# Kernel tuning notes

Hardware: AMD Instinct MI355X
Metric: run time of the kernel (lower is better)

Reference implementation:

```python
import jax, jax.numpy as jnp
import numpy as np

N = 100000
E = 1600000
F_IN, F_HID, F_OUT = 128, 256, 16


def gcn_conv(x, edge_index, W, b, num_nodes):
    """PyG-style GCNConv: out = D^{-1/2} (A + I) D^{-1/2} (x W) + b."""
    src, dst = edge_index[0], edge_index[1]
    # add self-loops
    loops = jnp.arange(num_nodes, dtype=edge_index.dtype)
    src = jnp.concatenate([src, loops])
    dst = jnp.concatenate([dst, loops])
    # degree of destination nodes (includes self-loop, so deg >= 1)
    deg = jax.ops.segment_sum(jnp.ones_like(dst, dtype=x.dtype), dst, num_segments=num_nodes)
    dinv = jax.lax.rsqrt(deg)
    norm = dinv[src] * dinv[dst]  # [E+N]
    h = x @ W                      # [N, out]  dense transform first (PyG order)
    msg = h[src] * norm[:, None]   # gather + scale, [E+N, out]
    out = jax.ops.segment_sum(msg, dst, num_segments=num_nodes)  # scatter-add
    return out + b


def setup_inputs() -> dict:
    key = jax.random.key(0)
    k1, k2, k3, k4 = jax.random.split(key, 4)
    x = jax.random.normal(k1, (N, F_IN), dtype=jnp.float32)
    edge_index = jax.random.randint(k2, (2, E), 0, N, dtype=jnp.int64)
    # Glorot-ish init for weights
    W1 = jax.random.normal(k3, (F_IN, F_HID), dtype=jnp.float32) / np.sqrt(F_IN)
    W2 = jax.random.normal(k4, (F_HID, F_OUT), dtype=jnp.float32) / np.sqrt(F_HID)
    b1 = jnp.zeros((F_HID,), dtype=jnp.float32)
    b2 = jnp.zeros((F_OUT,), dtype=jnp.float32)
    return {"x": x, "edge_index": edge_index, "W1": W1, "b1": b1, "W2": W2, "b2": b2}


def reference(x, edge_index, W1, b1, W2, b2):
    h = gcn_conv(x, edge_index, W1, b1, N)
    h = jax.nn.relu(h)
    # dropout p=0.5 is identity in eval mode
    h = gcn_conv(h, edge_index, W2, b2, N)
    return jax.nn.log_softmax(h, axis=1)
```

## Files before the change

kernel.cpp:

```cpp
#include <hip/hip_runtime.h>
#include <hip/hip_bf16.h>

#define F_IN   128
#define F_HID  256
#define F_OUT  16
#define NCH    256
#define MAXBUK 1600

__device__ inline unsigned short f2bf(float x) {
    unsigned int u = __float_as_uint(x);
    unsigned int r = (u + 0x7FFFu + ((u >> 16) & 1u)) >> 16;
    return (unsigned short)r;
}
__device__ inline unsigned int pack2(float lo, float hi) {
    return (unsigned int)f2bf(lo) | ((unsigned int)f2bf(hi) << 16);
}
__device__ inline void unpack8(uint4 v, float* f) {
    f[0] = __uint_as_float(v.x << 16); f[1] = __uint_as_float(v.x & 0xFFFF0000u);
    f[2] = __uint_as_float(v.y << 16); f[3] = __uint_as_float(v.y & 0xFFFF0000u);
    f[4] = __uint_as_float(v.z << 16); f[5] = __uint_as_float(v.z & 0xFFFF0000u);
    f[6] = __uint_as_float(v.w << 16); f[7] = __uint_as_float(v.w & 0xFFFF0000u);
}

__global__ __launch_bounds__(256) void hist_k(const int* __restrict__ ei,
                                              int* __restrict__ M,
                                              int E, int cpe, int nbuk) {
    __shared__ int h[MAXBUK];
    int tid = threadIdx.x, blk = blockIdx.x;
    for (int b = tid; b < nbuk; b += 256) h[b] = 0;
    __syncthreads();
    int e0 = blk * cpe;
    for (int i = tid; i < cpe; i += 256) {
        int e = e0 + i;
        if (e < E) atomicAdd(&h[ei[E + e] >> 6], 1);
    }
    __syncthreads();
    for (int b = tid; b < nbuk; b += 256) M[(size_t)blk * nbuk + b] = h[b];
}

__global__ __launch_bounds__(64) void colscan_k(int* __restrict__ M,
                                                int* __restrict__ totals,
                                                int nbuk) {
    int b = blockIdx.x, l = threadIdx.x;
    int v[4], s = 0;
    #pragma unroll
    for (int u = 0; u < 4; ++u) { v[u] = M[(size_t)(l * 4 + u) * nbuk + b]; s += v[u]; }
    int incl = s;
    #pragma unroll
    for (int o = 1; o < 64; o <<= 1) { int t = __shfl_up(incl, o); if (l >= o) incl += t; }
    int run = incl - s;
    #pragma unroll
    for (int u = 0; u < 4; ++u) { M[(size_t)(l * 4 + u) * nbuk + b] = run; run += v[u]; }
    if (l == 63) totals[b] = incl;
}

__global__ __launch_bounds__(1024) void base_k(const int* __restrict__ totals,
                                               int* __restrict__ base, int nbuk) {
    __shared__ int sm[1024];
    int t = threadIdx.x;
    int v0 = (2 * t     < nbuk) ? totals[2 * t]     : 0;
    int v1 = (2 * t + 1 < nbuk) ? totals[2 * t + 1] : 0;
    int p = v0 + v1;
    sm[t] = p;
    __syncthreads();
    for (int o = 1; o < 1024; o <<= 1) {
        int x = (t >= o) ? sm[t - o] : 0;
        __syncthreads();
        sm[t] += x;
        __syncthreads();
    }
    int excl = sm[t] - p;
    if (2 * t     < nbuk) base[2 * t]     = excl;
    if (2 * t + 1 < nbuk) base[2 * t + 1] = excl + v0;
}

__global__ __launch_bounds__(256) void bscatter_k(const int* __restrict__ ei,
                                                  const int* __restrict__ M,
                                                  const int* __restrict__ base,
                                                  int2* __restrict__ tmp,
                                                  int E, int cpe, int nbuk) {
    __shared__ int cur[MAXBUK];
    int tid = threadIdx.x, blk = blockIdx.x;
    for (int b = tid; b < nbuk; b += 256)
        cur[b] = base[b] + M[(size_t)blk * nbuk + b];
    __syncthreads();
    int e0 = blk * cpe;
    for (int i = tid; i < cpe; i += 256) {
        int e = e0 + i;
        if (e < E) {
            int s = ei[e], d = ei[E + e];
            int slot = atomicAdd(&cur[d >> 6], 1);
            tmp[slot] = make_int2(s, d);
        }
    }
}

__global__ __launch_bounds__(256) void fin_k(const int2* __restrict__ tmp,
                                             const int* __restrict__ base,
                                             const int* __restrict__ totals,
                                             const float* __restrict__ x,
                                             int* __restrict__ csr_src,
                                             int* __restrict__ start,
                                             int* __restrict__ deg,
                                             float* __restrict__ dinv,
                                             uint4* __restrict__ xs,
                                             int N) {
    __shared__ int dcnt[64], dcur[64];
    __shared__ float sdv[64];
    int b = blockIdx.x, tid = threadIdx.x;
    int bb = base[b], cnt = totals[b];
    if (tid < 64) dcnt[tid] = 0;
    __syncthreads();
    for (int i = tid; i < cnt; i += 256)
        atomicAdd(&dcnt[tmp[bb + i].y & 63], 1);
    __syncthreads();
    if (tid < 64) {
        int l = tid, v = dcnt[l];
        int incl = v;
        #pragma unroll
        for (int o = 1; o < 64; o <<= 1) { int t2 = __shfl_up(incl, o); if (l >= o) incl += t2; }
        int excl = incl - v;
        dcur[l] = excl;
        float dv = rsqrtf((float)v + 1.f);
        sdv[l] = dv;
        int d = b * 64 + l;
        if (d < N) { deg[d] = v; start[d] = bb + excl; dinv[d] = dv; }
    }
    __syncthreads();
    for (int i = tid; i < cnt; i += 256) {
        int2 p = tmp[bb + i];
        int r = atomicAdd(&dcur[p.y & 63], 1);
        csr_src[bb + r] = p.x;
    }
    int d0 = b * 64;
    int nn = min(64, N - d0);
    const float4* x4 = (const float4*)x;
    for (int i = tid; i < nn * 16; i += 256) {
        int l = i >> 4, c = i & 15;
        float dv = sdv[l];
        size_t f4i = (size_t)(d0 + l) * 32 + c * 2;
        float4 a = x4[f4i], bq = x4[f4i + 1];
        a.x *= dv; a.y *= dv; a.z *= dv; a.w *= dv;
        bq.x *= dv; bq.y *= dv; bq.z *= dv; bq.w *= dv;
        uint4 o;
        o.x = pack2(a.x, a.y);  o.y = pack2(a.z, a.w);
        o.z = pack2(bq.x, bq.y); o.w = pack2(bq.z, bq.w);
        xs[(size_t)(d0 + l) * 16 + c] = o;
    }
}

__global__ __launch_bounds__(256) void agg1_k(const uint4* __restrict__ xs,
                                              const float* __restrict__ dinv,
                                              const int* __restrict__ start,
                                              const int* __restrict__ deg,
                                              const int* __restrict__ csr_src,
                                              float* __restrict__ agg1,
                                              int N) {
    int wid = (blockIdx.x * 256 + threadIdx.x) >> 6;
    if (wid >= N) return;
    int lane = threadIdx.x & 63;
    int q  = lane >> 4;
    int li = lane & 15;

    float acc[8];
    {
        uint4 self = xs[(size_t)wid * 16 + li];
        float f[8]; unpack8(self, f);
        float sw = (q == 0) ? 1.f : 0.f;
        #pragma unroll
        for (int j = 0; j < 8; ++j) acc[j] = f[j] * sw;
    }

    int s0 = start[wid], cnt = deg[wid];
    for (int p = 0; p < cnt; p += 16) {
        int s[4]; float nm[4]; uint4 v[4];
        #pragma unroll
        for (int u = 0; u < 4; ++u) {
            int e = p + u * 4 + q;
            s[u]  = (e < cnt) ? csr_src[s0 + e] : wid;
            nm[u] = (e < cnt) ? 1.f : 0.f;
        }
        #pragma unroll
        for (int u = 0; u < 4; ++u)
            v[u] = xs[(size_t)s[u] * 16 + li];
        #pragma unroll
        for (int u = 0; u < 4; ++u) {
            float f[8]; unpack8(v[u], f);
            #pragma unroll
            for (int j = 0; j < 8; ++j) acc[j] = fmaf(f[j], nm[u], acc[j]);
        }
    }
    #pragma unroll
    for (int j = 0; j < 8; ++j) {
        acc[j] += __shfl_xor(acc[j], 16);
        acc[j] += __shfl_xor(acc[j], 32);
    }
    if (q == 0) {
        float dv = dinv[wid];
        float4 o0 = { acc[0] * dv, acc[1] * dv, acc[2] * dv, acc[3] * dv };
        float4 o1 = { acc[4] * dv, acc[5] * dv, acc[6] * dv, acc[7] * dv };
        ((float4*)agg1)[(size_t)wid * 32 + li * 2 + 0] = o0;
        ((float4*)agg1)[(size_t)wid * 32 + li * 2 + 1] = o1;
    }
}

#define BM 64
#define BN 64
#define BK 16

__global__ __launch_bounds__(256) void gemm1_relu_k(const float* __restrict__ A,
                                                    const float* __restrict__ B,
                                                    const float* __restrict__ bias,
                                                    float* __restrict__ C,
                                                    int M_) {
    __shared__ float As[BK][BM + 4];
    __shared__ float Bs[BK][BN + 4];
    int m0 = blockIdx.x * BM;
    int n0 = blockIdx.y * BN;
    int tid = threadIdx.x;
    int tx = tid & 15, ty = tid >> 4;
    float acc[4][4] = {};

    for (int k0 = 0; k0 < F_IN; k0 += BK) {
        {
            int r = tid >> 2, kk = (tid & 3) * 4;
            int row = m0 + r; if (row >= M_) row = M_ - 1;
            float4 av = *reinterpret_cast<const float4*>(A + (size_t)row * F_IN + k0 + kk);
            As[kk + 0][r] = av.x; As[kk + 1][r] = av.y;
            As[kk + 2][r] = av.z; As[kk + 3][r] = av.w;
        }
        {
            int k = tid >> 4, nn = (tid & 15) * 4;
            float4 bv = *reinterpret_cast<const float4*>(B + (size_t)(k0 + k) * F_HID + n0 + nn);
            *reinterpret_cast<float4*>(&Bs[k][nn]) = bv;
        }
        __syncthreads();
        #pragma unroll
        for (int kk = 0; kk < BK; ++kk) {
            float4 a = *reinterpret_cast<const float4*>(&As[kk][ty * 4]);
            float4 b = *reinterpret_cast<const float4*>(&Bs[kk][tx * 4]);
            acc[0][0] += a.x * b.x; acc[0][1] += a.x * b.y; acc[0][2] += a.x * b.z; acc[0][3] += a.x * b.w;
            acc[1][0] += a.y * b.x; acc[1][1] += a.y * b.y; acc[1][2] += a.y * b.z; acc[1][3] += a.y * b.w;
            acc[2][0] += a.z * b.x; acc[2][1] += a.z * b.y; acc[2][2] += a.z * b.z; acc[2][3] += a.z * b.w;
            acc[3][0] += a.w * b.x; acc[3][1] += a.w * b.y; acc[3][2] += a.w * b.z; acc[3][3] += a.w * b.w;
        }
        __syncthreads();
    }
    #pragma unroll
    for (int i = 0; i < 4; ++i) {
        int row = m0 + ty * 4 + i;
        if (row < M_) {
            float4 bi = *reinterpret_cast<const float4*>(bias + n0 + tx * 4);
            float4 o;
            o.x = fmaxf(acc[i][0] + bi.x, 0.f);
            o.y = fmaxf(acc[i][1] + bi.y, 0.f);
            o.z = fmaxf(acc[i][2] + bi.z, 0.f);
            o.w = fmaxf(acc[i][3] + bi.w, 0.f);
            *reinterpret_cast<float4*>(C + (size_t)row * F_HID + n0 + tx * 4) = o;
        }
    }
}

__global__ __launch_bounds__(256) void gemm2_k(const float* __restrict__ h1,
                                               const float* __restrict__ W2,
                                               const float* __restrict__ dinv,
                                               float* __restrict__ h2,
                                               int N) {
    __shared__ float w2s[F_HID * F_OUT];
    __shared__ float hs[16][F_HID + 4];
    int tid = threadIdx.x;
    const float4* wg = (const float4*)W2;
    float4* ws4 = (float4*)w2s;
    for (int i = tid; i < F_HID * F_OUT / 4; i += 256) ws4[i] = wg[i];
    int n0 = blockIdx.x * 16;
    const float4* hg = (const float4*)(h1 + (size_t)n0 * F_HID);
    for (int i = tid; i < 16 * F_HID / 4; i += 256) {
        int r = i >> 6, c = i & 63;
        *reinterpret_cast<float4*>(&hs[r][c * 4]) = hg[i];
    }
    __syncthreads();
    int ln = tid >> 4, j = tid & 15;
    float acc = 0.f;
    #pragma unroll 8
    for (int k = 0; k < F_HID; ++k) acc += hs[ln][k] * w2s[k * F_OUT + j];
    h2[(size_t)(n0 + ln) * F_OUT + j] = acc * dinv[n0 + ln];
}

__global__ __launch_bounds__(256) void agg2_softmax_k(const float* __restrict__ h2,
                                                      const float* __restrict__ dinv,
                                                      const int* __restrict__ start,
                                                      const int* __restrict__ deg,
                                                      const int* __restrict__ csr_src,
                                                      const float* __restrict__ b2,
                                                      float* __restrict__ out,
                                                      int N) {
    int wid = (blockIdx.x * 256 + threadIdx.x) >> 6;
    if (wid >= N) return;
    int lane = threadIdx.x & 63;
    int g  = lane >> 2;
    int j4 = lane & 3;
    const float4* h4 = (const float4*)h2;

    float sw = (g == 0) ? 1.f : 0.f;
    float4 self = h4[(size_t)wid * 4 + j4];
    float4 acc = { self.x * sw, self.y * sw, self.z * sw, self.w * sw };

    int s0 = start[wid], cnt = deg[wid];
    for (int p = 0; p < cnt; p += 16) {
        int e = p + g;
        bool ok = e < cnt;
        int   s  = ok ? csr_src[s0 + e] : wid;
        float nm = ok ? 1.f : 0.f;
        float4 v = h4[(size_t)s * 4 + j4];
        acc.x = fmaf(v.x, nm, acc.x);
        acc.y = fmaf(v.y, nm, acc.y);
        acc.z = fmaf(v.z, nm, acc.z);
        acc.w = fmaf(v.w, nm, acc.w);
    }
    #pragma unroll
    for (int o = 4; o <= 32; o <<= 1) {
        acc.x += __shfl_xor(acc.x, o);
        acc.y += __shfl_xor(acc.y, o);
        acc.z += __shfl_xor(acc.z, o);
        acc.w += __shfl_xor(acc.w, o);
    }
    float dv = dinv[wid];
    float4 bb = ((const float4*)b2)[j4];
    acc.x = acc.x * dv + bb.x; acc.y = acc.y * dv + bb.y;
    acc.z = acc.z * dv + bb.z; acc.w = acc.w * dv + bb.w;

    float m = fmaxf(fmaxf(acc.x, acc.y), fmaxf(acc.z, acc.w));
    m = fmaxf(m, __shfl_xor(m, 1));
    m = fmaxf(m, __shfl_xor(m, 2));
    float es = expf(acc.x - m) + expf(acc.y - m) + expf(acc.z - m) + expf(acc.w - m);
    es += __shfl_xor(es, 1);
    es += __shfl_xor(es, 2);
    float lse = m + logf(es);

    if (g == 0) {
        float4 o4 = { acc.x - lse, acc.y - lse, acc.z - lse, acc.w - lse };
        ((float4*)out)[(size_t)wid * 4 + j4] = o4;
    }
}

extern "C" void kernel_launch(void* const* d_in, const int* in_sizes, int n_in,
                              void* d_out, int out_size, void* d_ws, size_t ws_size,
                              hipStream_t stream) {
    const float* x  = (const float*)d_in[0];
    const int*   ei = (const int*)d_in[1];
    const float* W1 = (const float*)d_in[2];
    const float* b1 = (const float*)d_in[3];
    const float* W2 = (const float*)d_in[4];
    const float* b2 = (const float*)d_in[5];
    float* out = (float*)d_out;

    const int N = in_sizes[0] / F_IN;
    const int E = in_sizes[1] / 2;
    const int nbuk = (N + 63) >> 6;
    const int cpe  = (E + NCH - 1) / NCH;

    auto align4k = [](size_t v) { return (v + 4095) & ~(size_t)4095; };
    char* ws = (char*)d_ws;
    size_t off = 0;
    int*   M      = (int*)(ws + off);  off += align4k((size_t)NCH * nbuk * 4);
    int*   totals = (int*)(ws + off);  off += align4k((size_t)nbuk * 4);
    int*   base   = (int*)(ws + off);  off += align4k((size_t)nbuk * 4);
    int*   deg    = (int*)(ws + off);  off += align4k((size_t)N * 4);
    int*   start  = (int*)(ws + off);  off += align4k((size_t)N * 4);
    float* dinv   = (float*)(ws + off); off += align4k((size_t)N * 4);
    int*   csr    = (int*)(ws + off);  off += align4k((size_t)E * 4);
    float* agg1   = (float*)(ws + off); off += align4k((size_t)N * F_IN * 4);
    char*  R1     = ws + off;
    int2*  tmp    = (int2*)R1;
    uint4* xs     = (uint4*)(R1 + align4k((size_t)E * 8));
    float* h1     = (float*)R1;
    float* h2pre  = agg1;

    hist_k    <<<NCH, 256, 0, stream>>>(ei, M, E, cpe, nbuk);
    colscan_k <<<nbuk, 64, 0, stream>>>(M, totals, nbuk);
    base_k    <<<1, 1024, 0, stream>>>(totals, base, nbuk);
    bscatter_k<<<NCH, 256, 0, stream>>>(ei, M, base, tmp, E, cpe, nbuk);
    fin_k     <<<nbuk, 256, 0, stream>>>(tmp, base, totals, x, csr, start, deg,
                                         dinv, xs, N);

    agg1_k<<<(N + 3) / 4, 256, 0, stream>>>(xs, dinv, start, deg, csr, agg1, N);
    dim3 g1((N + BM - 1) / BM, F_HID / BN);
    gemm1_relu_k<<<g1, 256, 0, stream>>>(agg1, W1, b1, h1, N);

    gemm2_k<<<N / 16, 256, 0, stream>>>(h1, W2, dinv, h2pre, N);
    agg2_softmax_k<<<(N + 3) / 4, 256, 0, stream>>>(h2pre, dinv, start, deg,
                                                    csr, b2, out, N);
}
```

Before: 421.4 us.

## Replace fp32 SIMT GEMM1 with bf16 MFMA kernel and bf16 intermediates

Replaces the fp32 shared-memory tiled GEMM for layer 1 with a bf16 MFMA (16x16x32) kernel. W1 is staged transposed in LDS with an XOR swizzle, and A fragments are held in registers. agg1 and h1 are now stored as bf16 instead of fp32, roughly halving the memory traffic between agg1, gemm1 and gemm2. The trade is lower precision in the intermediates. The h1 stores are scalar 2-byte writes, which may be poorly coalesced.

New measurement: 344.7 us. 1.22x faster.

```diff
diff --git a/kernel.cpp b/kernel.cpp
--- a/kernel.cpp
+++ b/kernel.cpp
@@ -6,6 +6,9 @@
 #define F_OUT  16
 #define NCH    256
 #define MAXBUK 1600
+
+typedef float v4f __attribute__((ext_vector_type(4)));
+typedef short v8s __attribute__((ext_vector_type(8)));
 
 __device__ inline unsigned short f2bf(float x) {
     unsigned int u = __float_as_uint(x);
@@ -154,7 +157,7 @@
                                               const int* __restrict__ start,
                                               const int* __restrict__ deg,
                                               const int* __restrict__ csr_src,
-                                              float* __restrict__ agg1,
+                                              uint4* __restrict__ agg1bf,
                                               int N) {
     int wid = (blockIdx.x * 256 + threadIdx.x) >> 6;
     if (wid >= N) return;
@@ -197,71 +200,79 @@
     }
     if (q == 0) {
         float dv = dinv[wid];
-        float4 o0 = { acc[0] * dv, acc[1] * dv, acc[2] * dv, acc[3] * dv };
-        float4 o1 = { acc[4] * dv, acc[5] * dv, acc[6] * dv, acc[7] * dv };
-        ((float4*)agg1)[(size_t)wid * 32 + li * 2 + 0] = o0;
-        ((float4*)agg1)[(size_t)wid * 32 + li * 2 + 1] = o1;
-    }
-}
-
-#define BM 64
-#define BN 64
-#define BK 16
-
-__global__ __launch_bounds__(256) void gemm1_relu_k(const float* __restrict__ A,
-                                                    const float* __restrict__ B,
-                                                    const float* __restrict__ bias,
-                                                    float* __restrict__ C,
-                                                    int M_) {
-    __shared__ float As[BK][BM + 4];
-    __shared__ float Bs[BK][BN + 4];
-    int m0 = blockIdx.x * BM;
-    int n0 = blockIdx.y * BN;
+        uint4 o;
+        o.x = pack2(acc[0] * dv, acc[1] * dv);
+        o.y = pack2(acc[2] * dv, acc[3] * dv);
+        o.z = pack2(acc[4] * dv, acc[5] * dv);
+        o.w = pack2(acc[6] * dv, acc[7] * dv);
+        agg1bf[(size_t)wid * 16 + li] = o;
+    }
+}
+
+__global__ __launch_bounds__(256) void gemm1_mfma_k(
+        const unsigned short* __restrict__ A,
+        const float* __restrict__ W1,
+        const float* __restrict__ b1,
+        unsigned short* __restrict__ h1,
+        int N_) {
+    __shared__ unsigned short w1t[256 * 128];
     int tid = threadIdx.x;
-    int tx = tid & 15, ty = tid >> 4;
-    float acc[4][4] = {};
-
-    for (int k0 = 0; k0 < F_IN; k0 += BK) {
-        {
-            int r = tid >> 2, kk = (tid & 3) * 4;
-            int row = m0 + r; if (row >= M_) row = M_ - 1;
-            float4 av = *reinterpret_cast<const float4*>(A + (size_t)row * F_IN + k0 + kk);
-            As[kk + 0][r] = av.x; As[kk + 1][r] = av.y;
-            As[kk + 2][r] = av.z; As[kk + 3][r] = av.w;
+
+    for (int i = tid; i < 64 * 256; i += 256) {
+        int kk = i >> 8;
+        int n  = i & 255;
+        int k2 = kk << 1;
+        float w0 = W1[(size_t)k2 * 256 + n];
+        float w1v = W1[(size_t)(k2 + 1) * 256 + n];
+        int g = k2 >> 3;
+        unsigned int byteoff = (unsigned)n * 256u + ((unsigned)(g ^ (n & 15)) << 4) + ((unsigned)(k2 & 7) << 1);
+        *(unsigned int*)((char*)w1t + byteoff) = pack2(w0, w1v);
+    }
+    __syncthreads();
+
+    int w  = tid >> 6, l = tid & 63;
+    int lr = l & 15, kc = l >> 4;
+    int m0 = blockIdx.x * 256 + w * 64;
+
+    v8s a[4][4];
+    #pragma unroll
+    for (int rt = 0; rt < 4; ++rt) {
+        int row = m0 + rt * 16 + lr;
+        if (row >= N_) row = N_ - 1;
+        const unsigned short* ap = A + (size_t)row * 128 + kc * 8;
+        #pragma unroll
+        for (int kt = 0; kt < 4; ++kt)
+            a[rt][kt] = *(const v8s*)(ap + kt * 32);
+    }
+
+    for (int nt = 0; nt < 16; ++nt) {
+        const char* wb = (const char*)w1t + (unsigned)(nt * 16 + lr) * 256u;
+        v8s b0 = *(const v8s*)(wb + (((0 * 4 + kc) ^ lr) << 4));
+        v8s bb1 = *(const v8s*)(wb + (((1 * 4 + kc) ^ lr) << 4));
+        v8s b2 = *(const v8s*)(wb + (((2 * 4 + kc) ^ lr) << 4));
+        v8s b3 = *(const v8s*)(wb + (((3 * 4 + kc) ^ lr) << 4));
+        float bias = b1[nt * 16 + lr];
+        int colg = nt * 16 + lr;
+        #pragma unroll
+        for (int rt = 0; rt < 4; ++rt) {
+            v4f acc = {0.f, 0.f, 0.f, 0.f};
+            acc = __builtin_amdgcn_mfma_f32_16x16x32_bf16(a[rt][0], b0,  acc, 0, 0, 0);
+            acc = __builtin_amdgcn_mfma_f32_16x16x32_bf16(a[rt][1], bb1, acc, 0, 0, 0);
+            acc = __builtin_amdgcn_mfma_f32_16x16x32_bf16(a[rt][2], b2,  acc, 0, 0, 0);
+            acc = __builtin_amdgcn_mfma_f32_16x16x32_bf16(a[rt][3], b3,  acc, 0, 0, 0);
+            #pragma unroll
+            for (int r = 0; r < 4; ++r) {
+                int row = m0 + rt * 16 + kc * 4 + r;
+                if (row < N_) {
+                    float vv = fmaxf(acc[r] + bias, 0.f);
+                    h1[(size_t)row * 256 + colg] = f2bf(vv);
+                }
+            }
         }
-        {
-            int k = tid >> 4, nn = (tid & 15) * 4;
-            float4 bv = *reinterpret_cast<const float4*>(B + (size_t)(k0 + k) * F_HID + n0 + nn);
-            *reinterpret_cast<float4*>(&Bs[k][nn]) = bv;
-        }
-        __syncthreads();
-        #pragma unroll
-        for (int kk = 0; kk < BK; ++kk) {
-            float4 a = *reinterpret_cast<const float4*>(&As[kk][ty * 4]);
-            float4 b = *reinterpret_cast<const float4*>(&Bs[kk][tx * 4]);
-            acc[0][0] += a.x * b.x; acc[0][1] += a.x * b.y; acc[0][2] += a.x * b.z; acc[0][3] += a.x * b.w;
-            acc[1][0] += a.y * b.x; acc[1][1] += a.y * b.y; acc[1][2] += a.y * b.z; acc[1][3] += a.y * b.w;
-            acc[2][0] += a.z * b.x; acc[2][1] += a.z * b.y; acc[2][2] += a.z * b.z; acc[2][3] += a.z * b.w;
-            acc[3][0] += a.w * b.x; acc[3][1] += a.w * b.y; acc[3][2] += a.w * b.z; acc[3][3] += a.w * b.w;
-        }
-        __syncthreads();
-    }
-    #pragma unroll
-    for (int i = 0; i < 4; ++i) {
-        int row = m0 + ty * 4 + i;
-        if (row < M_) {
-            float4 bi = *reinterpret_cast<const float4*>(bias + n0 + tx * 4);
-            float4 o;
-            o.x = fmaxf(acc[i][0] + bi.x, 0.f);
-            o.y = fmaxf(acc[i][1] + bi.y, 0.f);
-            o.z = fmaxf(acc[i][2] + bi.z, 0.f);
-            o.w = fmaxf(acc[i][3] + bi.w, 0.f);
-            *reinterpret_cast<float4*>(C + (size_t)row * F_HID + n0 + tx * 4) = o;
-        }
-    }
-}
-
-__global__ __launch_bounds__(256) void gemm2_k(const float* __restrict__ h1,
+    }
+}
+
+__global__ __launch_bounds__(256) void gemm2_k(const unsigned short* __restrict__ h1,
                                                const float* __restrict__ W2,
                                                const float* __restrict__ dinv,
                                                float* __restrict__ h2,
@@ -273,10 +284,12 @@
     float4* ws4 = (float4*)w2s;
     for (int i = tid; i < F_HID * F_OUT / 4; i += 256) ws4[i] = wg[i];
     int n0 = blockIdx.x * 16;
-    const float4* hg = (const float4*)(h1 + (size_t)n0 * F_HID);
-    for (int i = tid; i < 16 * F_HID / 4; i += 256) {
-        int r = i >> 6, c = i & 63;
-        *reinterpret_cast<float4*>(&hs[r][c * 4]) = hg[i];
+    const uint4* hg = (const uint4*)(h1 + (size_t)n0 * F_HID);
+    for (int i = tid; i < 512; i += 256) {
+        int r = i >> 5, c = i & 31;
+        float f[8]; unpack8(hg[i], f);
+        #pragma unroll
+        for (int j = 0; j < 8; ++j) hs[r][c * 8 + j] = f[j];
     }
     __syncthreads();
     int ln = tid >> 4, j = tid & 15;
@@ -369,12 +382,13 @@
     int*   start  = (int*)(ws + off);  off += align4k((size_t)N * 4);
     float* dinv   = (float*)(ws + off); off += align4k((size_t)N * 4);
     int*   csr    = (int*)(ws + off);  off += align4k((size_t)E * 4);
-    float* agg1   = (float*)(ws + off); off += align4k((size_t)N * F_IN * 4);
+    char*  aggslot = ws + off;          off += align4k((size_t)N * F_IN * 4);
+    uint4* agg1bf = (uint4*)aggslot;
+    float* h2pre  = (float*)aggslot;
     char*  R1     = ws + off;
     int2*  tmp    = (int2*)R1;
     uint4* xs     = (uint4*)(R1 + align4k((size_t)E * 8));
-    float* h1     = (float*)R1;
-    float* h2pre  = agg1;
+    unsigned short* h1 = (unsigned short*)R1;
 
     hist_k    <<<NCH, 256, 0, stream>>>(ei, M, E, cpe, nbuk);
     colscan_k <<<nbuk, 64, 0, stream>>>(M, totals, nbuk);
@@ -383,9 +397,9 @@
     fin_k     <<<nbuk, 256, 0, stream>>>(tmp, base, totals, x, csr, start, deg,
                                          dinv, xs, N);
 
-    agg1_k<<<(N + 3) / 4, 256, 0, stream>>>(xs, dinv, start, deg, csr, agg1, N);
-    dim3 g1((N + BM - 1) / BM, F_HID / BN);
-    gemm1_relu_k<<<g1, 256, 0, stream>>>(agg1, W1, b1, h1, N);
+    agg1_k<<<(N + 3) / 4, 256, 0, stream>>>(xs, dinv, start, deg, csr, agg1bf, N);
+    gemm1_mfma_k<<<(N + 255) / 256, 256, 0, stream>>>(
+        (const unsigned short*)agg1bf, W1, b1, h1, N);
 
     gemm2_k<<<N / 16, 256, 0, stream>>>(h1, W2, dinv, h2pre, N);
     agg2_softmax_k<<<(N + 3) / 4, 256, 0, stream>>>(h2pre, dinv, start, deg,
```
